# Kernel optimization log

Hardware: AMD Instinct MI355X
Metric: run time of the kernel (lower is better)

The kernel has to match this reference:

```python
import jax, jax.numpy as jnp
import numpy as np

CHANNELS = 512
NUM_HEADS = 8
GROUPS = 32
EPS = 1e-5  # torch GroupNorm default


def setup_inputs() -> dict:
    key = jax.random.key(0)
    ks = jax.random.split(key, 7)
    B, C, H, W = 16, CHANNELS, 64, 64
    x = jax.random.normal(ks[0], (B, C, H, W), dtype=jnp.float32)
    # GroupNorm affine params (torch init: weight=1, bias=0; randomize slightly for a nontrivial baseline)
    gamma = jnp.ones((C,), jnp.float32) + 0.02 * jax.random.normal(ks[1], (C,), jnp.float32)
    beta = 0.02 * jax.random.normal(ks[2], (C,), jnp.float32)
    # 1x1 convs == dense matrices over channel dim
    w_qkv = jax.random.normal(ks[3], (3 * C, C), jnp.float32) / np.sqrt(C)
    b_qkv = 0.01 * jax.random.normal(ks[4], (3 * C,), jnp.float32)
    w_proj = jax.random.normal(ks[5], (C, C), jnp.float32) / np.sqrt(C)
    b_proj = 0.01 * jax.random.normal(ks[6], (C,), jnp.float32)
    return {"x": x, "gamma": gamma, "beta": beta, "w_qkv": w_qkv,
            "b_qkv": b_qkv, "w_proj": w_proj, "b_proj": b_proj}


def _group_norm(x, gamma, beta):
    B, C, H, W = x.shape
    xg = x.reshape(B, GROUPS, C // GROUPS, H, W)
    mean = jnp.mean(xg, axis=(2, 3, 4), keepdims=True)
    var = jnp.mean(jnp.square(xg - mean), axis=(2, 3, 4), keepdims=True)
    xn = ((xg - mean) * jax.lax.rsqrt(var + EPS)).reshape(B, C, H, W)
    return xn * gamma[:, None, None] + beta[:, None, None]


def reference(x, gamma, beta, w_qkv, b_qkv, w_proj, b_proj):
    B, C, H, W = x.shape
    h = NUM_HEADS
    d = C // h  # head_dim
    residual = x
    xn = _group_norm(x, gamma, beta)
    # 1x1 conv == per-pixel dense layer over channels
    qkv = jnp.einsum('bchw,oc->bohw', xn, w_qkv) + b_qkv[:, None, None]
    q, k, v = jnp.split(qkv, 3, axis=1)
    N = H * W
    # rearrange 'b (h c) h1 w1 -> b h c (h1 w1)': rows = head_dim, cols = spatial
    q = q.reshape(B, h, d, N)
    k = k.reshape(B, h, d, N)
    v = v.reshape(B, h, d, N)
    scale = d ** (-0.5)
    # attention over head_dim axis (faithful to the source rearrange)
    attn = jax.nn.softmax(jnp.einsum('bhcn,bhdn->bhcd', q, k) * scale, axis=-1)  # [B,h,d,d]
    out = jnp.einsum('bhcd,bhdn->bhcn', attn, v).reshape(B, C, H, W)
    out = jnp.einsum('bchw,oc->bohw', out, w_proj) + b_proj[:, None, None]
    return out + residual
```

## Files before the change

kernel.cpp:

```cpp
#include <hip/hip_runtime.h>

typedef unsigned short u16;
typedef __attribute__((ext_vector_type(8))) short short8;
typedef __attribute__((ext_vector_type(4))) float floatx4;
typedef __attribute__((ext_vector_type(4))) unsigned int uintx4;

#define B_    16
#define C_    512
#define N_    4096
#define NH_   8
#define HD_   64
#define MQKV  1536
#define NSPL  8

union V16 { uintx4 u; u16 s[8]; short8 h; };

__device__ inline u16 f2bf(float f) {
  union { float f; unsigned int i; } c; c.f = f;
  unsigned int i = c.i;
  return (u16)((i + 0x7FFFu + ((i >> 16) & 1u)) >> 16);
}

__device__ __forceinline__ void gld16(const u16* g, u16* l) {
  __builtin_amdgcn_global_load_lds(
      (const __attribute__((address_space(1))) unsigned int*)g,
      (__attribute__((address_space(3))) unsigned int*)l, 16, 0, 0);
}

__global__ __launch_bounds__(256) void gn_stats_t(const float* __restrict__ x,
    const float* __restrict__ gamma, const float* __restrict__ beta,
    float* __restrict__ s_arr, float* __restrict__ t_arr,
    u16* __restrict__ xtg, int b0) {
  __shared__ float T[16][256];
  int bl = blockIdx.x >> 5, g = blockIdx.x & 31;
  int gb = b0 + bl;
  int tid = threadIdx.x;
  const float* xb = x + ((size_t)bl * C_ + g * 16) * N_;
  u16* xd = xtg + ((size_t)bl * 32 + g) * N_ * 16;
  float sum = 0.f, ssq = 0.f;
  for (int t8 = 0; t8 < 16; ++t8) {
    int nb = t8 * 256;
#pragma unroll
    for (int i = 0; i < 4; ++i) {
      int idx = tid + i * 256;
      int row = idx >> 6, col4 = idx & 63;
      floatx4 v = *(const floatx4*)(xb + (size_t)row * N_ + nb + col4 * 4);
#pragma unroll
      for (int j = 0; j < 4; ++j) { float f = v[j]; sum += f; ssq += f * f; }
      *(floatx4*)&T[row][col4 * 4] = v;
    }
    __syncthreads();
    V16 a, b;
#pragma unroll
    for (int j = 0; j < 8; ++j) a.s[j] = f2bf(T[j][tid]);
#pragma unroll
    for (int j = 0; j < 8; ++j) b.s[j] = f2bf(T[8 + j][tid]);
    uintx4* dst = (uintx4*)(xd + (size_t)(nb + tid) * 16);
    dst[0] = a.u; dst[1] = b.u;
    __syncthreads();
  }
#pragma unroll
  for (int off = 32; off > 0; off >>= 1) {
    sum += __shfl_down(sum, off);
    ssq += __shfl_down(ssq, off);
  }
  __shared__ float red[8];
  __shared__ float mv[2];
  int lane = tid & 63, wid = tid >> 6;
  if (lane == 0) { red[wid] = sum; red[wid + 4] = ssq; }
  __syncthreads();
  if (tid == 0) {
    float s = red[0] + red[1] + red[2] + red[3];
    float q = red[4] + red[5] + red[6] + red[7];
    float mean = s * (1.f / 65536.f);
    float var  = q * (1.f / 65536.f) - mean * mean;
    mv[0] = mean; mv[1] = rsqrtf(var + 1e-5f);
  }
  __syncthreads();
  if (tid < 16) {
    int c = g * 16 + tid;
    float ga = gamma[c], be = beta[c];
    float mean = mv[0], rstd = mv[1];
    s_arr[gb * C_ + c] = ga * rstd;
    t_arr[gb * C_ + c] = be - mean * rstd * ga;
  }
}

__global__ __launch_bounds__(256) void cvt_bf16(const float* __restrict__ src,
                                                u16* __restrict__ dst) {
  int i = blockIdx.x * 256 + threadIdx.x;
  const floatx4* s4 = (const floatx4*)src;
  floatx4 a = s4[2 * i], b = s4[2 * i + 1];
  V16 v;
#pragma unroll
  for (int j = 0; j < 4; ++j) { v.s[j] = f2bf(a[j]); v.s[4 + j] = f2bf(b[j]); }
  ((uintx4*)dst)[i] = v.u;
}

__global__ __launch_bounds__(256) void fold_w(const float* __restrict__ w_qkv,
    const float* __restrict__ b_qkv, const float* __restrict__ s_arr,
    const float* __restrict__ t_arr, u16* __restrict__ wq2,
    float* __restrict__ bq2, int b0) {
  int bl = blockIdx.y, gb = b0 + bl;
  int o = blockIdx.x * 16 + (threadIdx.x >> 4);
  int cth = threadIdx.x & 15;
  const float* w  = w_qkv + (size_t)o * C_;
  const float* sp = s_arr + (size_t)gb * C_;
  const float* tp = t_arr + (size_t)gb * C_;
  u16* wd = wq2 + ((size_t)bl * MQKV + o) * C_;
  V16 buf[4];
  float bt = 0.f;
#pragma unroll
  for (int i = 0; i < 8; ++i) {
    int c = cth * 32 + i * 4;
    floatx4 wv = *(const floatx4*)(w + c);
    floatx4 sv = *(const floatx4*)(sp + c);
    floatx4 tv = *(const floatx4*)(tp + c);
#pragma unroll
    for (int j = 0; j < 4; ++j) {
      buf[i >> 1].s[(i & 1) * 4 + j] = f2bf(wv[j] * sv[j]);
      bt += wv[j] * tv[j];
    }
  }
  uintx4* wo = (uintx4*)(wd + cth * 32);
#pragma unroll
  for (int i = 0; i < 4; ++i) wo[i] = buf[i].u;
#pragma unroll
  for (int off = 8; off > 0; off >>= 1) bt += __shfl_xor(bt, off);
  if (cth == 0) bq2[(size_t)bl * MQKV + o] = b_qkv[o] + bt;
}

__global__ __launch_bounds__(256) void gemm_qkv(
    const u16* __restrict__ Wq, const u16* __restrict__ Xg,
    const float* __restrict__ bq2, u16* __restrict__ outp, int M) {
  __shared__ alignas(16) u16 smem[2 * 2 * 128 * 64];
  int bz = blockIdx.z;
  int m0 = blockIdx.y * 128, n0 = blockIdx.x * 128;
  int tid = threadIdx.x, lane = tid & 63, wid = tid >> 6;
  int quad = lane >> 4, l15 = lane & 15;
  int wm = (wid >> 1) * 64, wn = (wid & 1) * 64;
  int sr = tid >> 3, sc = tid & 7;
  const u16* Ab = Wq + (size_t)bz * ((size_t)M * C_);
  const u16* Bb = Xg + (size_t)bz * ((size_t)C_ * N_);
  const float* bias = bq2 + (size_t)bz * M;
  floatx4 acc[4][4];
#pragma unroll
  for (int i = 0; i < 4; ++i)
#pragma unroll
    for (int j = 0; j < 4; ++j) acc[i][j] = (floatx4)0.f;

  auto stage = [&](int kt, int p) {
    u16* As = smem + p * 16384;
    u16* Bs = As + 8192;
#pragma unroll
    for (int i = 0; i < 4; ++i) {
      int rr = sr + i * 32;
      int cc = sc ^ (rr & 7);
      gld16(Ab + (size_t)(m0 + rr) * C_ + kt * 64 + cc * 8, &As[rr * 64 + sc * 8]);
      gld16(Bb + ((size_t)(kt * 4 + (cc >> 1)) * N_ + n0 + rr) * 16 + (cc & 1) * 8,
            &Bs[rr * 64 + sc * 8]);
    }
  };

  stage(0, 0);
  asm volatile("s_waitcnt vmcnt(0)" ::: "memory");
  __builtin_amdgcn_s_barrier();
  int cur = 0;
  for (int kt = 0; kt < 8; ++kt) {
    if (kt < 7) stage(kt + 1, cur ^ 1);
    const u16* As = smem + cur * 16384;
    const u16* Bs = As + 8192;
#pragma unroll
    for (int ks = 0; ks < 2; ++ks) {
      short8 af[4], bf8[4];
#pragma unroll
      for (int mi = 0; mi < 4; ++mi) {
        int row = wm + mi * 16 + l15;
        int kc = (ks * 4 + quad) ^ (row & 7);
        af[mi] = *(const short8*)&As[row * 64 + kc * 8];
      }
#pragma unroll
      for (int ni = 0; ni < 4; ++ni) {
        int row = wn + ni * 16 + l15;
        int kc = (ks * 4 + quad) ^ (row & 7);
        bf8[ni] = *(const short8*)&Bs[row * 64 + kc * 8];
      }
#pragma unroll
      for (int mi = 0; mi < 4; ++mi)
#pragma unroll
        for (int ni = 0; ni < 4; ++ni)
          acc[mi][ni] = __builtin_amdgcn_mfma_f32_16x16x32_bf16(af[mi], bf8[ni], acc[mi][ni], 0, 0, 0);
    }
    asm volatile("s_waitcnt vmcnt(0)" ::: "memory");
    __builtin_amdgcn_s_barrier();
    cur ^= 1;
  }
  u16* E = smem;
#pragma unroll
  for (int mi = 0; mi < 4; ++mi)
#pragma unroll
    for (int ni = 0; ni < 4; ++ni)
#pragma unroll
      for (int r = 0; r < 4; ++r) {
        int row = wm + mi * 16 + quad * 4 + r;
        int col = wn + ni * 16 + l15;
        int ch = col >> 3;
        int cs = (ch & 8) | ((ch & 7) ^ (row & 7));
        E[row * 128 + cs * 8 + (col & 7)] = f2bf(acc[mi][ni][r] + bias[m0 + row]);
      }
  __syncthreads();
  int row = tid >> 1, half = tid & 1;
  u16* orow = outp + ((size_t)bz * M + m0 + row) * N_ + n0 + half * 64;
#pragma unroll
  for (int k = 0; k < 8; ++k) {
    int cs = (half * 8) | (k ^ (row & 7));
    *(uintx4*)(orow + k * 8) = *(const uintx4*)&E[row * 128 + cs * 8];
  }
}

__global__ __launch_bounds__(256) void gemm_bt(
    const u16* __restrict__ A, const u16* __restrict__ Bm,
    const float* __restrict__ bias, const float* __restrict__ resid,
    float* __restrict__ outv, int M) {
  __shared__ alignas(16) u16 smem[2 * 2 * 128 * 64];
  int bz = blockIdx.z;
  int m0 = blockIdx.y * 128, n0 = blockIdx.x * 128;
  int tid = threadIdx.x, lane = tid & 63, wid = tid >> 6;
  int quad = lane >> 4, l15 = lane & 15;
  int wm = (wid >> 1) * 64, wn = (wid & 1) * 64;
  int sr = tid >> 3, sc = tid & 7;
  const u16* Bb = Bm + (size_t)bz * ((size_t)N_ * C_);
  floatx4 acc[4][4];
#pragma unroll
  for (int i = 0; i < 4; ++i)
#pragma unroll
    for (int j = 0; j < 4; ++j) acc[i][j] = (floatx4)0.f;

  auto stage = [&](int kt, int p) {
    u16* As = smem + p * 16384;
    u16* Bs = As + 8192;
#pragma unroll
    for (int i = 0; i < 4; ++i) {
      int rr = sr + i * 32;
      int cc = sc ^ (rr & 7);
      gld16(A  + (size_t)(m0 + rr) * C_ + kt * 64 + cc * 8, &As[rr * 64 + sc * 8]);
      gld16(Bb + (size_t)(n0 + rr) * C_ + kt * 64 + cc * 8, &Bs[rr * 64 + sc * 8]);
    }
  };

  stage(0, 0);
  asm volatile("s_waitcnt vmcnt(0)" ::: "memory");
  __builtin_amdgcn_s_barrier();
  int cur = 0;
  for (int kt = 0; kt < 8; ++kt) {
    if (kt < 7) stage(kt + 1, cur ^ 1);
    const u16* As = smem + cur * 16384;
    const u16* Bs = As + 8192;
#pragma unroll
    for (int ks = 0; ks < 2; ++ks) {
      short8 af[4], bf8[4];
#pragma unroll
      for (int mi = 0; mi < 4; ++mi) {
        int row = wm + mi * 16 + l15;
        int kc = (ks * 4 + quad) ^ (row & 7);
        af[mi] = *(const short8*)&As[row * 64 + kc * 8];
      }
#pragma unroll
      for (int ni = 0; ni < 4; ++ni) {
        int row = wn + ni * 16 + l15;
        int kc = (ks * 4 + quad) ^ (row & 7);
        bf8[ni] = *(const short8*)&Bs[row * 64 + kc * 8];
      }
#pragma unroll
      for (int mi = 0; mi < 4; ++mi)
#pragma unroll
        for (int ni = 0; ni < 4; ++ni)
          acc[mi][ni] = __builtin_amdgcn_mfma_f32_16x16x32_bf16(af[mi], bf8[ni], acc[mi][ni], 0, 0, 0);
    }
    asm volatile("s_waitcnt vmcnt(0)" ::: "memory");
    __builtin_amdgcn_s_barrier();
    cur ^= 1;
  }
  float* E = (float*)smem;
#pragma unroll
  for (int p = 0; p < 2; ++p) {
#pragma unroll
    for (int q = 0; q < 2; ++q)
#pragma unroll
      for (int ni = 0; ni < 4; ++ni)
#pragma unroll
        for (int r = 0; r < 4; ++r) {
          int mi = p * 2 + q;
          int lr = (wid >> 1) * 32 + q * 16 + quad * 4 + r;
          int col = wn + ni * 16 + l15;
          int ch = col >> 2;
          int cs = (ch & ~7) | ((ch & 7) ^ (lr & 7));
          E[lr * 128 + cs * 4 + (col & 3)] =
              acc[mi][ni][r] + bias[m0 + wm + mi * 16 + quad * 4 + r];
        }
    __syncthreads();
    int lr = tid >> 2, qt = tid & 3;
    int o = m0 + (lr >> 5) * 64 + p * 32 + (lr & 31);
    size_t obase = ((size_t)bz * M + o) * N_ + n0 + qt * 4;
#pragma unroll
    for (int k = 0; k < 8; ++k) {
      int ch = k * 4 + qt;
      int cs = (ch & ~7) | ((ch & 7) ^ (lr & 7));
      floatx4 v = *(const floatx4*)&E[lr * 128 + cs * 4];
      v += *(const floatx4*)(resid + obase + (size_t)k * 16);
      *(floatx4*)(outv + obase + (size_t)k * 16) = v;
    }
    if (p == 0) __syncthreads();
  }
}

__global__ __launch_bounds__(256) void qk_partial(const u16* __restrict__ qkv,
    float* __restrict__ spart, int nbh) {
  int h = blockIdx.x, bz = blockIdx.y, p = blockIdx.z;
  const u16* qb = qkv + ((size_t)bz * MQKV + h * HD_) * N_;
  const u16* kb = qkv + ((size_t)bz * MQKV + C_ + h * HD_) * N_;
  int tid = threadIdx.x, lane = tid & 63, wid = tid >> 6;
  int quad = lane >> 4, l15 = lane & 15;
  floatx4 acc[4][4];
#pragma unroll
  for (int i = 0; i < 4; ++i)
#pragma unroll
    for (int j = 0; j < 4; ++j) acc[i][j] = (floatx4)0.f;

  for (int ks = 0; ks < 4; ++ks) {
    int n = p * 512 + wid * 128 + ks * 32 + quad * 8;
    short8 af[4], bf8[4];
#pragma unroll
    for (int mi = 0; mi < 4; ++mi)
      af[mi] = *(const short8*)(qb + (size_t)(mi * 16 + l15) * N_ + n);
#pragma unroll
    for (int ni = 0; ni < 4; ++ni)
      bf8[ni] = *(const short8*)(kb + (size_t)(ni * 16 + l15) * N_ + n);
#pragma unroll
    for (int mi = 0; mi < 4; ++mi)
#pragma unroll
      for (int ni = 0; ni < 4; ++ni)
        acc[mi][ni] = __builtin_amdgcn_mfma_f32_16x16x32_bf16(af[mi], bf8[ni], acc[mi][ni], 0, 0, 0);
  }
  __shared__ float S[64 * 68];
  for (int i = tid; i < 64 * 68; i += 256) S[i] = 0.f;
  __syncthreads();
#pragma unroll
  for (int mi = 0; mi < 4; ++mi)
#pragma unroll
    for (int ni = 0; ni < 4; ++ni)
#pragma unroll
      for (int r = 0; r < 4; ++r)
        atomicAdd(&S[(mi * 16 + quad * 4 + r) * 68 + ni * 16 + l15], acc[mi][ni][r]);
  __syncthreads();
  int bh = bz * NH_ + h;
  float* dst = spart + ((size_t)p * nbh + bh) * 4096 + tid * 16;
  int row = tid >> 2, c0 = (tid & 3) * 16;
#pragma unroll
  for (int j = 0; j < 4; ++j)
    *(floatx4*)(dst + j * 4) = *(const floatx4*)&S[row * 68 + c0 + j * 4];
}

__global__ __launch_bounds__(64) void softmax_rows(const float* __restrict__ spart,
    float* __restrict__ attn, int nbh) {
  int bh = blockIdx.x, c = threadIdx.x;
  const float* sp = spart + (size_t)bh * 4096 + c * 64;
  floatx4 row4[16];
#pragma unroll
  for (int j = 0; j < 16; ++j) row4[j] = *(const floatx4*)(sp + j * 4);
#pragma unroll
  for (int p = 1; p < NSPL; ++p) {
    const float* spp = sp + (size_t)p * nbh * 4096;
#pragma unroll
    for (int j = 0; j < 16; ++j) row4[j] += *(const floatx4*)(spp + j * 4);
  }
  float mx = -1e30f;
#pragma unroll
  for (int j = 0; j < 16; ++j)
#pragma unroll
    for (int e = 0; e < 4; ++e) mx = fmaxf(mx, row4[j][e]);
  float sum = 0.f;
#pragma unroll
  for (int j = 0; j < 16; ++j)
#pragma unroll
    for (int e = 0; e < 4; ++e) {
      float ev = __expf((row4[j][e] - mx) * 0.125f);
      row4[j][e] = ev; sum += ev;
    }
  float inv = 1.f / sum;
  float* dst = attn + (size_t)bh * 4096 + c * 64;
#pragma unroll
  for (int j = 0; j < 16; ++j) *(floatx4*)(dst + j * 4) = row4[j] * inv;
}

__global__ __launch_bounds__(256) void pv_kernel(const float* __restrict__ attn,
    const u16* __restrict__ qkv, u16* __restrict__ ot) {
  int nt = blockIdx.x, h = blockIdx.y, bz = blockIdx.z;
  int n0 = nt * 256;
  const u16* vb = qkv + ((size_t)bz * MQKV + 2 * C_ + h * HD_) * N_;
  __shared__ alignas(16) u16 Ps[64 * 72];
  __shared__ alignas(16) u16 Vs[256 * 72];
  int tid = threadIdx.x, lane = tid & 63, wid = tid >> 6;
  int quad = lane >> 4, l15 = lane & 15;
  const float* ab = attn + (size_t)(bz * NH_ + h) * 4096;
#pragma unroll
  for (int i = 0; i < 16; ++i) {
    int idx = tid + i * 256;
    int row = idx >> 6, col = idx & 63;
    Ps[row * 72 + col] = f2bf(ab[idx]);
  }
#pragma unroll
  for (int i = 0; i < 8; ++i) {
    int l = tid + i * 256;
    int ch = l >> 5, n8 = (l & 31) * 8;
    V16 v; v.u = *(const uintx4*)(vb + (size_t)ch * N_ + n0 + n8);
    int chunk = ch >> 3, clo = ch & 7;
#pragma unroll
    for (int j = 0; j < 8; ++j) {
      int nl = n8 + j;
      Vs[nl * 72 + (chunk ^ ((nl >> 3) & 7)) * 8 + clo] = v.s[j];
    }
  }
  __syncthreads();
  floatx4 acc[4][4];
#pragma unroll
  for (int i = 0; i < 4; ++i)
#pragma unroll
    for (int j = 0; j < 4; ++j) acc[i][j] = (floatx4)0.f;
#pragma unroll
  for (int ks = 0; ks < 2; ++ks) {
    short8 af[4], bf8[4];
    int ko = ks * 32 + quad * 8;
#pragma unroll
    for (int mi = 0; mi < 4; ++mi)
      af[mi] = *(const short8*)&Ps[(mi * 16 + l15) * 72 + ko];
    int chunk = ks * 4 + quad;
#pragma unroll
    for (int ni = 0; ni < 4; ++ni) {
      int nl = wid * 64 + ni * 16 + l15;
      bf8[ni] = *(const short8*)&Vs[nl * 72 + (chunk ^ ((nl >> 3) & 7)) * 8];
    }
#pragma unroll
    for (int mi = 0; mi < 4; ++mi)
#pragma unroll
      for (int ni = 0; ni < 4; ++ni)
        acc[mi][ni] = __builtin_amdgcn_mfma_f32_16x16x32_bf16(af[mi], bf8[ni], acc[mi][ni], 0, 0, 0);
  }
  __syncthreads();
  u16* Ls = Vs;
#pragma unroll
  for (int mi = 0; mi < 4; ++mi)
#pragma unroll
    for (int ni = 0; ni < 4; ++ni)
#pragma unroll
      for (int r = 0; r < 4; ++r) {
        int n  = wid * 64 + ni * 16 + l15;
        int hd = mi * 16 + quad * 4 + r;
        Ls[n * 64 + (((hd >> 3) ^ (n & 7)) * 8) + (hd & 7)] = f2bf(acc[mi][ni][r]);
      }
  __syncthreads();
  uintx4* dst = (uintx4*)(ot + ((size_t)bz * N_ + n0 + tid) * C_ + h * HD_);
#pragma unroll
  for (int k = 0; k < 8; ++k) {
    int kc = k ^ (tid & 7);
    dst[k] = *(const uintx4*)&Ls[tid * 64 + kc * 8];
  }
}

extern "C" void kernel_launch(void* const* d_in, const int* in_sizes, int n_in,
                              void* d_out, int out_size, void* d_ws, size_t ws_size,
                              hipStream_t stream) {
  const float* x      = (const float*)d_in[0];
  const float* gamma  = (const float*)d_in[1];
  const float* beta   = (const float*)d_in[2];
  const float* w_qkv  = (const float*)d_in[3];
  const float* b_qkv  = (const float*)d_in[4];
  const float* w_proj = (const float*)d_in[5];
  const float* b_proj = (const float*)d_in[6];
  float* out = (float*)d_out;

  const size_t fixed = (size_t)2 * B_ * C_ * 4 + (size_t)C_ * C_ * 2;
  const size_t per_batch = (size_t)MQKV * 4 + (size_t)MQKV * C_ * 2 +
                           (size_t)NH_ * 4096 * 4 + (size_t)C_ * N_ * 2 +
                           (size_t)MQKV * N_ * 2;
  int Bc = 16;
  while (Bc > 1 && fixed + (size_t)Bc * per_batch > ws_size) Bc >>= 1;

  float* s_arr = (float*)d_ws;
  float* t_arr = s_arr + B_ * C_;
  u16* wp   = (u16*)(t_arr + B_ * C_);
  float* bq2 = (float*)(wp + (size_t)C_ * C_);
  u16* wq2  = (u16*)(bq2 + (size_t)Bc * MQKV);
  float* attn = (float*)(wq2 + (size_t)Bc * MQKV * C_);
  u16* xtg  = (u16*)(attn + (size_t)Bc * NH_ * 4096);
  u16* qkv  = xtg + (size_t)Bc * C_ * N_;
  float* spart = (float*)xtg;
  u16* ot = xtg;

  cvt_bf16<<<dim3(C_ * C_ / 2048), dim3(256), 0, stream>>>(w_proj, wp);

  for (int b0 = 0; b0 < B_; b0 += Bc) {
    int nbh = Bc * NH_;
    gn_stats_t<<<dim3(Bc * 32), dim3(256), 0, stream>>>(
        x + (size_t)b0 * C_ * N_, gamma, beta, s_arr, t_arr, xtg, b0);
    fold_w<<<dim3(MQKV / 16, Bc), dim3(256), 0, stream>>>(
        w_qkv, b_qkv, s_arr, t_arr, wq2, bq2, b0);
    gemm_qkv<<<dim3(32, 12, Bc), dim3(256), 0, stream>>>(
        wq2, xtg, bq2, qkv, MQKV);
    qk_partial<<<dim3(NH_, Bc, NSPL), dim3(256), 0, stream>>>(qkv, spart, nbh);
    softmax_rows<<<dim3(nbh), dim3(64), 0, stream>>>(spart, attn, nbh);
    pv_kernel<<<dim3(16, NH_, Bc), dim3(256), 0, stream>>>(attn, qkv, ot);
    gemm_bt<<<dim3(32, 4, Bc), dim3(256), 0, stream>>>(
        wp, ot, b_proj, x + (size_t)b0 * C_ * N_, out + (size_t)b0 * C_ * N_, C_);
  }
}
```

Measured before the change: 692.4 us.

## Fold attention matrix into projection weights, eliminating the PV GEMM

Replaces the per-pixel attn@V kernel with a small fold_attn kernel that multiplies the projection weights by the per-head attention matrix, giving a per-batch C×C weight W2. The QKV GEMM now writes V transposed (pixel-major), so the projection GEMM reads V directly as its B operand with per-batch strides. This removes the PV GEMM and its full-size intermediate write and read, at the cost of a per-batch weight fold and a transposed V epilogue. It also adds an extra bf16 rounding of the folded weights.

```diff
diff --git a/kernel.cpp b/kernel.cpp
--- a/kernel.cpp
+++ b/kernel.cpp
@@ -196,32 +196,56 @@
     cur ^= 1;
   }
   u16* E = smem;
-#pragma unroll
-  for (int mi = 0; mi < 4; ++mi)
-#pragma unroll
-    for (int ni = 0; ni < 4; ++ni)
-#pragma unroll
-      for (int r = 0; r < 4; ++r) {
-        int row = wm + mi * 16 + quad * 4 + r;
-        int col = wn + ni * 16 + l15;
-        int ch = col >> 3;
-        int cs = (ch & 8) | ((ch & 7) ^ (row & 7));
-        E[row * 128 + cs * 8 + (col & 7)] = f2bf(acc[mi][ni][r] + bias[m0 + row]);
-      }
-  __syncthreads();
-  int row = tid >> 1, half = tid & 1;
-  u16* orow = outp + ((size_t)bz * M + m0 + row) * N_ + n0 + half * 64;
-#pragma unroll
-  for (int k = 0; k < 8; ++k) {
-    int cs = (half * 8) | (k ^ (row & 7));
-    *(uintx4*)(orow + k * 8) = *(const uintx4*)&E[row * 128 + cs * 8];
+  if (m0 < 2 * C_) {
+#pragma unroll
+    for (int mi = 0; mi < 4; ++mi)
+#pragma unroll
+      for (int ni = 0; ni < 4; ++ni)
+#pragma unroll
+        for (int r = 0; r < 4; ++r) {
+          int row = wm + mi * 16 + quad * 4 + r;
+          int col = wn + ni * 16 + l15;
+          int ch = col >> 3;
+          int cs = (ch & 8) | ((ch & 7) ^ (row & 7));
+          E[row * 128 + cs * 8 + (col & 7)] = f2bf(acc[mi][ni][r] + bias[m0 + row]);
+        }
+    __syncthreads();
+    int row = tid >> 1, half = tid & 1;
+    u16* orow = outp + ((size_t)bz * M + m0 + row) * N_ + n0 + half * 64;
+#pragma unroll
+    for (int k = 0; k < 8; ++k) {
+      int cs = (half * 8) | (k ^ (row & 7));
+      *(uintx4*)(orow + k * 8) = *(const uintx4*)&E[row * 128 + cs * 8];
+    }
+  } else {
+#pragma unroll
+    for (int mi = 0; mi < 4; ++mi)
+#pragma unroll
+      for (int ni = 0; ni < 4; ++ni)
+#pragma unroll
+        for (int r = 0; r < 4; ++r) {
+          int cl = wm + mi * 16 + quad * 4 + r;
+          int nl = wn + ni * 16 + l15;
+          int ch = cl >> 3;
+          int cs = (ch & 8) | ((ch & 7) ^ (nl & 7));
+          E[nl * 128 + cs * 8 + (cl & 7)] = f2bf(acc[mi][ni][r] + bias[m0 + cl]);
+        }
+    __syncthreads();
+    u16* vt = outp + ((size_t)bz * M + 2 * C_) * N_;
+    int nl = tid >> 1, half = tid & 1;
+    u16* drow = vt + (size_t)(n0 + nl) * C_ + (m0 - 2 * C_) + half * 64;
+#pragma unroll
+    for (int k = 0; k < 8; ++k) {
+      int cs = (half * 8) | (k ^ (nl & 7));
+      *(uintx4*)(drow + k * 8) = *(const uintx4*)&E[nl * 128 + cs * 8];
+    }
   }
 }
 
 __global__ __launch_bounds__(256) void gemm_bt(
     const u16* __restrict__ A, const u16* __restrict__ Bm,
     const float* __restrict__ bias, const float* __restrict__ resid,
-    float* __restrict__ outv, int M) {
+    float* __restrict__ outv, int M, size_t astride, size_t bstride) {
   __shared__ alignas(16) u16 smem[2 * 2 * 128 * 64];
   int bz = blockIdx.z;
   int m0 = blockIdx.y * 128, n0 = blockIdx.x * 128;
@@ -229,7 +253,8 @@
   int quad = lane >> 4, l15 = lane & 15;
   int wm = (wid >> 1) * 64, wn = (wid & 1) * 64;
   int sr = tid >> 3, sc = tid & 7;
-  const u16* Bb = Bm + (size_t)bz * ((size_t)N_ * C_);
+  const u16* Ab = A + (size_t)bz * astride;
+  const u16* Bb = Bm + (size_t)bz * bstride;
   floatx4 acc[4][4];
 #pragma unroll
   for (int i = 0; i < 4; ++i)
@@ -243,7 +268,7 @@
     for (int i = 0; i < 4; ++i) {
       int rr = sr + i * 32;
       int cc = sc ^ (rr & 7);
-      gld16(A  + (size_t)(m0 + rr) * C_ + kt * 64 + cc * 8, &As[rr * 64 + sc * 8]);
+      gld16(Ab + (size_t)(m0 + rr) * C_ + kt * 64 + cc * 8, &As[rr * 64 + sc * 8]);
       gld16(Bb + (size_t)(n0 + rr) * C_ + kt * 64 + cc * 8, &Bs[rr * 64 + sc * 8]);
     }
   };
@@ -393,78 +418,56 @@
   for (int j = 0; j < 16; ++j) *(floatx4*)(dst + j * 4) = row4[j] * inv;
 }
 
-__global__ __launch_bounds__(256) void pv_kernel(const float* __restrict__ attn,
-    const u16* __restrict__ qkv, u16* __restrict__ ot) {
-  int nt = blockIdx.x, h = blockIdx.y, bz = blockIdx.z;
-  int n0 = nt * 256;
-  const u16* vb = qkv + ((size_t)bz * MQKV + 2 * C_ + h * HD_) * N_;
-  __shared__ alignas(16) u16 Ps[64 * 72];
-  __shared__ alignas(16) u16 Vs[256 * 72];
+__global__ __launch_bounds__(256) void fold_attn(const u16* __restrict__ wp,
+    const float* __restrict__ attn, u16* __restrict__ W2) {
+  __shared__ u16 AT[64 * 72];
+  int h = blockIdx.x, bz = blockIdx.y;
   int tid = threadIdx.x, lane = tid & 63, wid = tid >> 6;
   int quad = lane >> 4, l15 = lane & 15;
   const float* ab = attn + (size_t)(bz * NH_ + h) * 4096;
-#pragma unroll
-  for (int i = 0; i < 16; ++i) {
-    int idx = tid + i * 256;
-    int row = idx >> 6, col = idx & 63;
-    Ps[row * 72 + col] = f2bf(ab[idx]);
-  }
-#pragma unroll
-  for (int i = 0; i < 8; ++i) {
-    int l = tid + i * 256;
-    int ch = l >> 5, n8 = (l & 31) * 8;
-    V16 v; v.u = *(const uintx4*)(vb + (size_t)ch * N_ + n0 + n8);
-    int chunk = ch >> 3, clo = ch & 7;
-#pragma unroll
-    for (int j = 0; j < 8; ++j) {
-      int nl = n8 + j;
-      Vs[nl * 72 + (chunk ^ ((nl >> 3) & 7)) * 8 + clo] = v.s[j];
+  {
+    int d = tid >> 2, j0 = (tid & 3) * 16;
+#pragma unroll
+    for (int j4 = 0; j4 < 4; ++j4) {
+      floatx4 v = *(const floatx4*)(ab + (size_t)d * 64 + j0 + j4 * 4);
+#pragma unroll
+      for (int j = 0; j < 4; ++j) AT[(j0 + j4 * 4 + j) * 72 + d] = f2bf(v[j]);
     }
   }
   __syncthreads();
-  floatx4 acc[4][4];
-#pragma unroll
-  for (int i = 0; i < 4; ++i)
+  floatx4 acc[8][4];
+#pragma unroll
+  for (int i = 0; i < 8; ++i)
 #pragma unroll
     for (int j = 0; j < 4; ++j) acc[i][j] = (floatx4)0.f;
 #pragma unroll
   for (int ks = 0; ks < 2; ++ks) {
-    short8 af[4], bf8[4];
-    int ko = ks * 32 + quad * 8;
-#pragma unroll
-    for (int mi = 0; mi < 4; ++mi)
-      af[mi] = *(const short8*)&Ps[(mi * 16 + l15) * 72 + ko];
-    int chunk = ks * 4 + quad;
-#pragma unroll
-    for (int ni = 0; ni < 4; ++ni) {
-      int nl = wid * 64 + ni * 16 + l15;
-      bf8[ni] = *(const short8*)&Vs[nl * 72 + (chunk ^ ((nl >> 3) & 7)) * 8];
-    }
-#pragma unroll
-    for (int mi = 0; mi < 4; ++mi)
+    short8 af[8], bf8[4];
+#pragma unroll
+    for (int mi = 0; mi < 8; ++mi) {
+      int o = wid * 128 + mi * 16 + l15;
+      af[mi] = *(const short8*)(wp + (size_t)o * C_ + h * HD_ + ks * 32 + quad * 8);
+    }
+#pragma unroll
+    for (int ni = 0; ni < 4; ++ni)
+      bf8[ni] = *(const short8*)&AT[(ni * 16 + l15) * 72 + ks * 32 + quad * 8];
+#pragma unroll
+    for (int mi = 0; mi < 8; ++mi)
 #pragma unroll
       for (int ni = 0; ni < 4; ++ni)
         acc[mi][ni] = __builtin_amdgcn_mfma_f32_16x16x32_bf16(af[mi], bf8[ni], acc[mi][ni], 0, 0, 0);
   }
-  __syncthreads();
-  u16* Ls = Vs;
-#pragma unroll
-  for (int mi = 0; mi < 4; ++mi)
+  u16* W2b = W2 + (size_t)bz * C_ * C_;
+#pragma unroll
+  for (int mi = 0; mi < 8; ++mi)
 #pragma unroll
     for (int ni = 0; ni < 4; ++ni)
 #pragma unroll
       for (int r = 0; r < 4; ++r) {
-        int n  = wid * 64 + ni * 16 + l15;
-        int hd = mi * 16 + quad * 4 + r;
-        Ls[n * 64 + (((hd >> 3) ^ (n & 7)) * 8) + (hd & 7)] = f2bf(acc[mi][ni][r]);
+        int o  = wid * 128 + mi * 16 + quad * 4 + r;
+        int dp = ni * 16 + l15;
+        W2b[(size_t)o * C_ + h * HD_ + dp] = f2bf(acc[mi][ni][r]);
       }
-  __syncthreads();
-  uintx4* dst = (uintx4*)(ot + ((size_t)bz * N_ + n0 + tid) * C_ + h * HD_);
-#pragma unroll
-  for (int k = 0; k < 8; ++k) {
-    int kc = k ^ (tid & 7);
-    dst[k] = *(const uintx4*)&Ls[tid * 64 + kc * 8];
-  }
 }
 
 extern "C" void kernel_launch(void* const* d_in, const int* in_sizes, int n_in,
@@ -481,21 +484,21 @@
 
   const size_t fixed = (size_t)2 * B_ * C_ * 4 + (size_t)C_ * C_ * 2;
   const size_t per_batch = (size_t)MQKV * 4 + (size_t)MQKV * C_ * 2 +
-                           (size_t)NH_ * 4096 * 4 + (size_t)C_ * N_ * 2 +
-                           (size_t)MQKV * N_ * 2;
+                           (size_t)NH_ * 4096 * 4 + (size_t)C_ * C_ * 2 +
+                           (size_t)C_ * N_ * 2 + (size_t)MQKV * N_ * 2;
   int Bc = 16;
   while (Bc > 1 && fixed + (size_t)Bc * per_batch > ws_size) Bc >>= 1;
 
   float* s_arr = (float*)d_ws;
   float* t_arr = s_arr + B_ * C_;
-  u16* wp   = (u16*)(t_arr + B_ * C_);
+  u16* wp    = (u16*)(t_arr + B_ * C_);
   float* bq2 = (float*)(wp + (size_t)C_ * C_);
-  u16* wq2  = (u16*)(bq2 + (size_t)Bc * MQKV);
+  u16* wq2   = (u16*)(bq2 + (size_t)Bc * MQKV);
   float* attn = (float*)(wq2 + (size_t)Bc * MQKV * C_);
-  u16* xtg  = (u16*)(attn + (size_t)Bc * NH_ * 4096);
-  u16* qkv  = xtg + (size_t)Bc * C_ * N_;
+  u16* W2    = (u16*)(attn + (size_t)Bc * NH_ * 4096);
+  u16* xtg   = W2 + (size_t)Bc * C_ * C_;
+  u16* qkv   = xtg + (size_t)Bc * C_ * N_;
   float* spart = (float*)xtg;
-  u16* ot = xtg;
 
   cvt_bf16<<<dim3(C_ * C_ / 2048), dim3(256), 0, stream>>>(w_proj, wp);
 
@@ -509,8 +512,9 @@
         wq2, xtg, bq2, qkv, MQKV);
     qk_partial<<<dim3(NH_, Bc, NSPL), dim3(256), 0, stream>>>(qkv, spart, nbh);
     softmax_rows<<<dim3(nbh), dim3(64), 0, stream>>>(spart, attn, nbh);
-    pv_kernel<<<dim3(16, NH_, Bc), dim3(256), 0, stream>>>(attn, qkv, ot);
+    fold_attn<<<dim3(NH_, Bc), dim3(256), 0, stream>>>(wp, attn, W2);
     gemm_bt<<<dim3(32, 4, Bc), dim3(256), 0, stream>>>(
-        wp, ot, b_proj, x + (size_t)b0 * C_ * N_, out + (size_t)b0 * C_ * N_, C_);
-  }
-}
+        W2, qkv + (size_t)2 * C_ * N_, b_proj, x + (size_t)b0 * C_ * N_,
+        out + (size_t)b0 * C_ * N_, C_, (size_t)C_ * C_, (size_t)MQKV * N_);
+  }
+}
```

Measured after the change: 674.9 us. 1.03x faster.
